# Optimization experiments

Hardware: AMD Instinct MI355X
Metric: run time of the kernel (lower is better)

The kernel has to match this reference:

```python
import jax, jax.numpy as jnp
import numpy as np

H, D, L, G = 4, 32, 2, 512   # heads, head_dim, conv layers, num graphs
HC = H * D                    # hidden_channels = 128


def _mlp3(x, ws, bs):
    # PyG-style MLP, 3 layers, relu between (no act after last), dropout=0
    for i in range(3):
        x = x @ ws[i] + bs[i]
        if i < 2:
            x = jax.nn.relu(x)
    return x


def _attend(q_dst, k_src, v_src, edge, a_rel_et, m_rel_et, p_rel_et, n_dst):
    """One HGTConv edge-type: relation transform, per-dst segment softmax, scatter.
    q_dst: [Nd,H,D], k_src/v_src: [Ns,H,D], edge: [2,E] (src,dst)."""
    src, dst = edge[0], edge[1]
    k_t = jnp.einsum('nhd,hde->nhe', k_src, a_rel_et)   # relation-specific key
    v_t = jnp.einsum('nhd,hde->nhe', v_src, m_rel_et)   # relation-specific value
    alpha = (q_dst[dst] * k_t[src]).sum(-1) * p_rel_et / jnp.sqrt(jnp.float32(D))  # [E,H]
    amax = jax.ops.segment_max(alpha, dst, num_segments=n_dst)
    amax = jnp.where(jnp.isfinite(amax), amax, 0.0)      # nodes with no in-edges
    ex = jnp.exp(alpha - amax[dst])
    den = jax.ops.segment_sum(ex, dst, num_segments=n_dst)
    w = ex / den[dst]                                    # segment softmax weights
    out = jax.ops.segment_sum(v_t[src] * w[..., None], dst, num_segments=n_dst)
    return out.reshape(n_dst, HC)


def _forward(x_var, x_con, mlp_in_w, mlp_in_b,
             mlp_out_w0, mlp_out_b0, mlp_out_w1, mlp_out_b1, mlp_out_w2, mlp_out_b2,
             k_w, k_b, q_w, q_b, v_w, v_b, a_w, a_b, skip,
             a_rel, m_rel, p_rel, edge_vc, edge_cv, batch_var):
    Nv, Nc = x_var.shape[0], x_con.shape[0]
    # per-node-type input MLPs (nt 0 = variable, nt 1 = constraint)
    xs = [_mlp3(x_var, mlp_in_w[0], mlp_in_b[0]),
          _mlp3(x_con, mlp_in_w[1], mlp_in_b[1])]
    ns = [Nv, Nc]
    for l in range(L):  # HGTConv layers
        k = [(xs[t] @ k_w[l, t] + k_b[l, t]).reshape(ns[t], H, D) for t in (0, 1)]
        q = [(xs[t] @ q_w[l, t] + q_b[l, t]).reshape(ns[t], H, D) for t in (0, 1)]
        v = [(xs[t] @ v_w[l, t] + v_b[l, t]).reshape(ns[t], H, D) for t in (0, 1)]
        # edge type 0: variable -> constraint ; edge type 1: constraint -> variable
        agg_con = _attend(q[1], k[0], v[0], edge_vc, a_rel[l, 0], m_rel[l, 0], p_rel[l, 0], Nc)
        agg_var = _attend(q[0], k[1], v[1], edge_cv, a_rel[l, 1], m_rel[l, 1], p_rel[l, 1], Nv)
        # group='mean' over incoming edge types (one per dst type here), then a_lin + gated skip
        new_xs = []
        for t, agg in ((0, agg_var), (1, agg_con)):
            out = jax.nn.gelu(agg, approximate=False) @ a_w[l, t] + a_b[l, t]
            g = jax.nn.sigmoid(skip[l, t])
            new_xs.append(g * out + (1.0 - g) * xs[t])
        xs = new_xs
    # output head on 'variable' nodes: MLP -> softmax(dim=1) -> global mean pool
    logits = _mlp3(xs[0], [mlp_out_w0, mlp_out_w1, mlp_out_w2], [mlp_out_b0, mlp_out_b1, mlp_out_b2])
    probs = jax.nn.softmax(logits, axis=1)
    summ = jax.ops.segment_sum(probs, batch_var, num_segments=G)
    cnt = jax.ops.segment_sum(jnp.ones((xs[0].shape[0],), probs.dtype), batch_var, num_segments=G)
    return summ / jnp.maximum(cnt, 1.0)[:, None]


def setup_inputs() -> dict:
    key = jax.random.key(0)
    ks = jax.random.split(key, 24)
    Nv = Nc = 50000
    E = 400000
    s = 1.0 / np.sqrt(HC)  # fan-in scale for hidden-width linears
    sd = 1.0 / np.sqrt(D)
    inp = {
        'x_var': jax.random.normal(ks[0], (Nv, HC), jnp.float32),
        'x_con': jax.random.normal(ks[1], (Nc, HC), jnp.float32),
        'mlp_in_w': jax.random.normal(ks[2], (2, 3, HC, HC), jnp.float32) * s,
        'mlp_in_b': jnp.zeros((2, 3, HC), jnp.float32),
        'mlp_out_w0': jax.random.normal(ks[3], (HC, HC), jnp.float32) * s,
        'mlp_out_b0': jnp.zeros((HC,), jnp.float32),
        'mlp_out_w1': jax.random.normal(ks[4], (HC, HC), jnp.float32) * s,
        'mlp_out_b1': jnp.zeros((HC,), jnp.float32),
        'mlp_out_w2': jax.random.normal(ks[5], (HC, 2), jnp.float32) * s,
        'mlp_out_b2': jnp.zeros((2,), jnp.float32),
        'k_w': jax.random.normal(ks[6], (L, 2, HC, HC), jnp.float32) * s,
        'k_b': jnp.zeros((L, 2, HC), jnp.float32),
        'q_w': jax.random.normal(ks[7], (L, 2, HC, HC), jnp.float32) * s,
        'q_b': jnp.zeros((L, 2, HC), jnp.float32),
        'v_w': jax.random.normal(ks[8], (L, 2, HC, HC), jnp.float32) * s,
        'v_b': jnp.zeros((L, 2, HC), jnp.float32),
        'a_w': jax.random.normal(ks[9], (L, 2, HC, HC), jnp.float32) * s,
        'a_b': jnp.zeros((L, 2, HC), jnp.float32),
        'skip': jnp.ones((L, 2), jnp.float32),
        'a_rel': jax.random.normal(ks[10], (L, 2, H, D, D), jnp.float32) * sd,
        'm_rel': jax.random.normal(ks[11], (L, 2, H, D, D), jnp.float32) * sd,
        'p_rel': jnp.ones((L, 2, H), jnp.float32),
        'edge_vc': jnp.stack([jax.random.randint(ks[12], (E,), 0, Nv, jnp.int32),
                              jax.random.randint(ks[13], (E,), 0, Nc, jnp.int32)]),
        'edge_cv': jnp.stack([jax.random.randint(ks[14], (E,), 0, Nc, jnp.int32),
                              jax.random.randint(ks[15], (E,), 0, Nv, jnp.int32)]),
        'batch_var': jnp.sort(jax.random.randint(ks[16], (Nv,), 0, G, jnp.int32)),
    }
    return inp


def reference(x_var, x_con, mlp_in_w, mlp_in_b,
              mlp_out_w0, mlp_out_b0, mlp_out_w1, mlp_out_b1, mlp_out_w2, mlp_out_b2,
              k_w, k_b, q_w, q_b, v_w, v_b, a_w, a_b, skip,
              a_rel, m_rel, p_rel, edge_vc, edge_cv, batch_var):
    return _forward(x_var, x_con, mlp_in_w, mlp_in_b,
                    mlp_out_w0, mlp_out_b0, mlp_out_w1, mlp_out_b1, mlp_out_w2, mlp_out_b2,
                    k_w, k_b, q_w, q_b, v_w, v_b, a_w, a_b, skip,
                    a_rel, m_rel, p_rel, edge_vc, edge_cv, batch_var)
```

## Files before the change

kernel.cpp:

```cpp
#include <hip/hip_runtime.h>
#include <cstddef>
#include <cstdint>

typedef __attribute__((ext_vector_type(8))) short short8;
typedef __attribute__((ext_vector_type(4))) float float4v;
typedef __attribute__((ext_vector_type(2))) float float2v;
typedef __attribute__((ext_vector_type(2))) __bf16 bf162;

__device__ __forceinline__ float bf2f_lo(unsigned int u) {
    union { unsigned int i; float f; } v; v.i = u << 16; return v.f;
}
__device__ __forceinline__ float bf2f_hi(unsigned int u) {
    union { unsigned int i; float f; } v; v.i = u & 0xFFFF0000u; return v.f;
}
__device__ __forceinline__ unsigned short f2bf(float f) {
    union { float f; unsigned int i; } v; v.f = f;
    unsigned int x = v.i;
    unsigned int r = (x + 0x7FFFu + ((x >> 16) & 1u)) >> 16;
    return (unsigned short)r;
}
__device__ __forceinline__ float geluf(float x) {
    return 0.5f * x * (1.0f + erff(x * 0.70710678118654752f));
}
__device__ __forceinline__ float dot2bf(unsigned int a, unsigned int b, float c) {
#if defined(__has_builtin) && __has_builtin(__builtin_amdgcn_fdot2_f32_bf16)
    union U { unsigned int u; bf162 v; };
    U ua, ub; ua.u = a; ub.u = b;
    return __builtin_amdgcn_fdot2_f32_bf16(ua.v, ub.v, c, false);
#else
    return c + bf2f_lo(a) * bf2f_lo(b) + bf2f_hi(a) * bf2f_hi(b);
#endif
}
__device__ __forceinline__ unsigned int gate_pack(unsigned int nu, unsigned int ou,
                                                  float2v g2, float2v og2) {
    float2v n = {bf2f_lo(nu), bf2f_hi(nu)};
    float2v o = {bf2f_lo(ou), bf2f_hi(ou)};
    float2v r = n * g2 + o * og2;
    return (unsigned int)f2bf(r.x) | ((unsigned int)f2bf(r.y) << 16);
}

__global__ void k_zero(int* __restrict__ p, int n) {
    int i = blockIdx.x * 256 + threadIdx.x;
    if (i < n) p[i] = 0;
}

__global__ void k_swz(const float* __restrict__ mlp_in_w, const float* __restrict__ q_w,
                      const float* __restrict__ a_w, const float* __restrict__ mow0,
                      const float* __restrict__ mow1, const float* __restrict__ mow2,
                      const float* __restrict__ kw, const float* __restrict__ kb,
                      const float* __restrict__ vw, const float* __restrict__ vb,
                      const float* __restrict__ arel, const float* __restrict__ mrel,
                      const float* __restrict__ prel,
                      unsigned short* __restrict__ Wswz, float* __restrict__ Bkv) {
    int idx = blockIdx.y;
    int f = blockIdx.x * 256 + threadIdx.x;
    if (idx == 25) {
        if (f >= 1024) return;
        int lt = f >> 8, c = f & 255;
        int sec = c >> 7, cc = c & 127, h = cc >> 5, e = cc & 31;
        const float* B = sec ? vb : kb;
        const float* R = sec ? mrel : arel;
        float scale = sec ? 1.f : prel[lt * 4 + h] * 0.17677669529663687f;
        const float* rp = R + (size_t)(lt * 4 + h) * 1024 + e;
        const float* bp = B + lt * 128 + h * 32;
        float s = 0.f;
        #pragma unroll 8
        for (int d = 0; d < 32; ++d) s += bp[d] * rp[(size_t)d * 32];
        Bkv[lt * 256 + c] = s * scale;
        return;
    }
    if (f >= 16384) return;
    int j = f & 7, l = (f >> 3) & 63, t = (f >> 9) & 7, sb = f >> 12;
    int k = sb * 32 + (l >> 4) * 8 + j;
    int n = t * 16 + (l & 15);
    float val;
    if (idx < 6)        val = mlp_in_w[(size_t)idx * 16384 + (size_t)k * 128 + n];
    else if (idx < 10)  val = q_w[(size_t)(idx - 6) * 16384 + (size_t)k * 128 + n];
    else if (idx < 14)  val = a_w[(size_t)(idx - 10) * 16384 + (size_t)k * 128 + n];
    else if (idx == 14) val = mow0[(size_t)k * 128 + n];
    else if (idx == 15) val = mow1[(size_t)k * 128 + n];
    else if (idx < 24) {
        int u = idx - 16, lt = u >> 1, sec = u & 1;
        int h = n >> 5, e = n & 31;
        const float* W = sec ? vw : kw;
        const float* R = sec ? mrel : arel;
        float scale = sec ? 1.f : prel[lt * 4 + h] * 0.17677669529663687f;
        const float* rp = R + (size_t)(lt * 4 + h) * 1024 + e;
        const float* wp = W + (size_t)lt * 16384 + (size_t)k * 128 + h * 32;
        float s = 0.f;
        #pragma unroll 8
        for (int d = 0; d < 32; ++d) s += wp[d] * rp[(size_t)d * 32];
        val = s * scale;
    } else val = (n < 2) ? mow2[(size_t)k * 2 + n] : 0.f;
    Wswz[(size_t)idx * 16384 + f] = f2bf(val);
}

__device__ __forceinline__ void mfma32(const short8 av[4], const unsigned short* __restrict__ Bu,
                                       float4v acc[8]) {
    #pragma unroll
    for (int s = 0; s < 4; ++s)
        #pragma unroll
        for (int t = 0; t < 8; ++t) {
            short8 bv = *(const short8*)(Bu + (s * 8 + t) * 512);
            acc[t] = __builtin_amdgcn_mfma_f32_16x16x32_bf16(av[s], bv, acc[t], 0, 0, 0);
        }
}

__global__ __launch_bounds__(256) void k_mlp3qkv(
    const float* __restrict__ Xa, const float* __restrict__ Xb,
    const unsigned short* __restrict__ Wswz, const float* __restrict__ mlp_in_b,
    const float* __restrict__ q_b, const float* __restrict__ Bkv,
    unsigned short* __restrict__ curS, unsigned short* __restrict__ Qs,
    unsigned short* __restrict__ KVs, int NT, int Nv) {
    __shared__ unsigned short lds[4][16][136];
    const int lane = threadIdx.x & 63, wave = threadIdx.x >> 6;
    const int quad = lane >> 4, mrow = lane & 15;
    const int mbase = blockIdx.x * 64 + wave * 16;
    if (mbase >= NT) return;
    const bool first = mbase < Nv;
    const float* bs = mlp_in_b + (first ? 0 : 384);
    const int ub = first ? 0 : 3;
    const int lt = first ? 0 : 1;
    int r0 = mbase + mrow; if (r0 >= NT) r0 = NT - 1;
    const float* ap = ((r0 < Nv) ? (Xa + (size_t)r0 * 128)
                                 : (Xb + (size_t)(r0 - Nv) * 128)) + quad * 8;
    short8 av[4];
    #pragma unroll
    for (int s = 0; s < 4; ++s) {
        float4 f0 = *(const float4*)(ap + s * 32);
        float4 f1 = *(const float4*)(ap + s * 32 + 4);
        short8 a;
        a[0] = (short)f2bf(f0.x); a[1] = (short)f2bf(f0.y);
        a[2] = (short)f2bf(f0.z); a[3] = (short)f2bf(f0.w);
        a[4] = (short)f2bf(f1.x); a[5] = (short)f2bf(f1.y);
        a[6] = (short)f2bf(f1.z); a[7] = (short)f2bf(f1.w);
        av[s] = a;
    }
    #pragma unroll
    for (int layer = 0; layer < 3; ++layer) {
        const unsigned short* Bu = Wswz + (size_t)(ub + layer) * 16384 + lane * 8;
        float4v acc[8];
        #pragma unroll
        for (int t = 0; t < 8; ++t) acc[t] = (float4v){0.f, 0.f, 0.f, 0.f};
        mfma32(av, Bu, acc);
        const float* b = bs + layer * 128;
        bool relu = layer < 2;
        #pragma unroll
        for (int t = 0; t < 8; ++t) {
            int col = t * 16 + mrow;
            float bb = b[col];
            #pragma unroll
            for (int r = 0; r < 4; ++r) {
                float v = acc[t][r] + bb;
                if (relu) v = fmaxf(v, 0.f);
                lds[wave][quad * 4 + r][col] = f2bf(v);
            }
        }
        #pragma unroll
        for (int s = 0; s < 4; ++s)
            av[s] = *(const short8*)&lds[wave][mrow][s * 32 + quad * 8];
    }
    {
        int row = mbase + mrow;
        if (row < NT) {
            #pragma unroll
            for (int s = 0; s < 4; ++s)
                *(uint4*)(curS + (size_t)row * 128 + quad * 8 + s * 32) = *(uint4*)&av[s];
        }
    }
    #pragma unroll
    for (int u = 0; u < 3; ++u) {
        int unit = (u == 0) ? (6 + lt) : (16 + lt * 2 + (u - 1));
        const unsigned short* Bu = Wswz + (size_t)unit * 16384 + lane * 8;
        float4v acc[8];
        #pragma unroll
        for (int t = 0; t < 8; ++t) acc[t] = (float4v){0.f, 0.f, 0.f, 0.f};
        mfma32(av, Bu, acc);
        const float* bias = (u == 0) ? (q_b + lt * 128) : (Bkv + lt * 256 + (u - 1) * 128);
        unsigned short* C = (u == 0) ? Qs : KVs;
        const int ldC = (u == 0) ? 128 : 256;
        const int cb = (u == 0) ? 0 : (u - 1) * 128;
        #pragma unroll
        for (int t = 0; t < 8; ++t) {
            int col = t * 16 + mrow;
            float b = bias[col];
            #pragma unroll
            for (int r = 0; r < 4; ++r) {
                int row = mbase + quad * 4 + r;
                if (row < NT) C[(size_t)row * ldC + cb + col] = f2bf(acc[t][r] + b);
            }
        }
    }
}

__global__ __launch_bounds__(256) void k_alinqkv(
    const unsigned short* __restrict__ Aagg, const unsigned short* __restrict__ Wswz,
    const float* __restrict__ a_b, const float* __restrict__ skipP,
    const float* __restrict__ q_b, const float* __restrict__ Bkv,
    unsigned short* __restrict__ curS, unsigned short* __restrict__ Qs,
    unsigned short* __restrict__ KVs, int NT, int Nv, int l) {
    __shared__ unsigned short lds[4][16][136];
    const int lane = threadIdx.x & 63, wave = threadIdx.x >> 6;
    const int quad = lane >> 4, mrow = lane & 15;
    const int mbase = blockIdx.x * 64 + wave * 16;
    if (mbase >= NT) return;
    const int type = (mbase >= Nv) ? 1 : 0;
    const int ltA = l * 2 + type;
    const int ltQ = (l + 1) * 2 + type;
    int r0 = mbase + mrow; if (r0 >= NT) r0 = NT - 1;
    const unsigned short* ap = Aagg + (size_t)r0 * 128 + quad * 8;
    short8 av[4];
    #pragma unroll
    for (int s = 0; s < 4; ++s) av[s] = *(const short8*)(ap + s * 32);
    {
        const unsigned short* Bu = Wswz + (size_t)(10 + ltA) * 16384 + lane * 8;
        float4v acc[8];
        #pragma unroll
        for (int t = 0; t < 8; ++t) acc[t] = (float4v){0.f, 0.f, 0.f, 0.f};
        mfma32(av, Bu, acc);
        const float* b = a_b + ltA * 128;
        #pragma unroll
        for (int t = 0; t < 8; ++t) {
            int col = t * 16 + mrow;
            float bb = b[col];
            #pragma unroll
            for (int r = 0; r < 4; ++r)
                lds[wave][quad * 4 + r][col] = f2bf(acc[t][r] + bb);
        }
    }
    {
        float gg = 1.f / (1.f + __expf(-skipP[ltA]));
        float2v g2 = {gg, gg}, og2 = {1.f - gg, 1.f - gg};
        int row = mbase + mrow;
        bool ok = row < NT;
        size_t rbase = (size_t)(ok ? row : 0) * 128;
        #pragma unroll
        for (int s = 0; s < 4; ++s) {
            short8 nv = *(const short8*)&lds[wave][mrow][s * 32 + quad * 8];
            uint4 nu = *(uint4*)&nv;
            uint4 ou = *(const uint4*)(curS + rbase + quad * 8 + s * 32);
            uint4 res;
            res.x = gate_pack(nu.x, ou.x, g2, og2);
            res.y = gate_pack(nu.y, ou.y, g2, og2);
            res.z = gate_pack(nu.z, ou.z, g2, og2);
            res.w = gate_pack(nu.w, ou.w, g2, og2);
            if (ok) *(uint4*)(curS + (size_t)row * 128 + quad * 8 + s * 32) = res;
            av[s] = *(short8*)&res;
        }
    }
    #pragma unroll
    for (int u = 0; u < 3; ++u) {
        int unit = (u == 0) ? (6 + ltQ) : (16 + ltQ * 2 + (u - 1));
        const unsigned short* Bu = Wswz + (size_t)unit * 16384 + lane * 8;
        float4v acc[8];
        #pragma unroll
        for (int t = 0; t < 8; ++t) acc[t] = (float4v){0.f, 0.f, 0.f, 0.f};
        mfma32(av, Bu, acc);
        const float* bias = (u == 0) ? (q_b + ltQ * 128) : (Bkv + ltQ * 256 + (u - 1) * 128);
        unsigned short* C = (u == 0) ? Qs : KVs;
        const int ldC = (u == 0) ? 128 : 256;
        const int cb = (u == 0) ? 0 : (u - 1) * 128;
        #pragma unroll
        for (int t = 0; t < 8; ++t) {
            int col = t * 16 + mrow;
            float b = bias[col];
            #pragma unroll
            for (int r = 0; r < 4; ++r) {
                int row = mbase + quad * 4 + r;
                if (row < NT) C[(size_t)row * ldC + cb + col] = f2bf(acc[t][r] + b);
            }
        }
    }
}

__global__ __launch_bounds__(256) void k_alinhead(
    const unsigned short* __restrict__ Aagg, const unsigned short* __restrict__ Wswz,
    const float* __restrict__ a_b, const float* __restrict__ skipP,
    const unsigned short* __restrict__ curS,
    const float* __restrict__ mob0, const float* __restrict__ mob1,
    const float* __restrict__ mob2, const int* __restrict__ batch,
    int N, int G, float* __restrict__ gsum, float* __restrict__ gcnt) {
    __shared__ unsigned short lds[4][16][136];
    __shared__ float sb[64][3];
    const int lane = threadIdx.x & 63, wave = threadIdx.x >> 6;
    const int quad = lane >> 4, mrow = lane & 15;
    const int tix = threadIdx.x;
    for (int i = tix; i < 192; i += 256) ((float*)sb)[i] = 0.f;
    __syncthreads();
    const int mbase = blockIdx.x * 64 + wave * 16;
    int bbase = blockIdx.x * 64; if (bbase >= N) bbase = N - 1;
    const int bmin = batch[bbase];
    if (mbase < N) {
        int r0 = mbase + mrow; if (r0 >= N) r0 = N - 1;
        const unsigned short* ap = Aagg + (size_t)r0 * 128 + quad * 8;
        short8 av[4];
        #pragma unroll
        for (int s = 0; s < 4; ++s) av[s] = *(const short8*)(ap + s * 32);
        {
            const unsigned short* Bu = Wswz + (size_t)12 * 16384 + lane * 8;
            float4v acc[8];
            #pragma unroll
            for (int t = 0; t < 8; ++t) acc[t] = (float4v){0.f, 0.f, 0.f, 0.f};
            mfma32(av, Bu, acc);
            const float* b = a_b + 2 * 128;
            #pragma unroll
            for (int t = 0; t < 8; ++t) {
                int col = t * 16 + mrow;
                float bb = b[col];
                #pragma unroll
                for (int r = 0; r < 4; ++r)
                    lds[wave][quad * 4 + r][col] = f2bf(acc[t][r] + bb);
            }
        }
        {
            float gg = 1.f / (1.f + __expf(-skipP[2]));
            float2v g2 = {gg, gg}, og2 = {1.f - gg, 1.f - gg};
            size_t rbase = (size_t)r0 * 128;
            #pragma unroll
            for (int s = 0; s < 4; ++s) {
                short8 nv = *(const short8*)&lds[wave][mrow][s * 32 + quad * 8];
                uint4 nu = *(uint4*)&nv;
                uint4 ou = *(const uint4*)(curS + rbase + quad * 8 + s * 32);
                uint4 res;
                res.x = gate_pack(nu.x, ou.x, g2, og2);
                res.y = gate_pack(nu.y, ou.y, g2, og2);
                res.z = gate_pack(nu.z, ou.z, g2, og2);
                res.w = gate_pack(nu.w, ou.w, g2, og2);
                av[s] = *(short8*)&res;
            }
        }
        #pragma unroll
        for (int layer = 0; layer < 2; ++layer) {
            const unsigned short* Bu = Wswz + (size_t)(14 + layer) * 16384 + lane * 8;
            float4v acc[8];
            #pragma unroll
            for (int t = 0; t < 8; ++t) acc[t] = (float4v){0.f, 0.f, 0.f, 0.f};
            mfma32(av, Bu, acc);
            const float* b = layer ? mob1 : mob0;
            #pragma unroll
            for (int t = 0; t < 8; ++t) {
                int col = t * 16 + mrow;
                float bb = b[col];
                #pragma unroll
                for (int r = 0; r < 4; ++r)
                    lds[wave][quad * 4 + r][col] = f2bf(fmaxf(acc[t][r] + bb, 0.f));
            }
            #pragma unroll
            for (int s = 0; s < 4; ++s)
                av[s] = *(const short8*)&lds[wave][mrow][s * 32 + quad * 8];
        }
        float4v lg = (float4v){0.f, 0.f, 0.f, 0.f};
        #pragma unroll
        for (int s = 0; s < 4; ++s) {
            short8 bv = *(const short8*)(Wswz + (size_t)24 * 16384 + (size_t)(s * 8) * 512 + lane * 8);
            lg = __builtin_amdgcn_mfma_f32_16x16x32_bf16(av[s], bv, lg, 0, 0, 0);
        }
        float4v lgo;
        #pragma unroll
        for (int r = 0; r < 4; ++r) lgo[r] = __shfl_xor(lg[r], 1);
        if (mrow == 0) {
            #pragma unroll
            for (int r = 0; r < 4; ++r) {
                int row = mbase + quad * 4 + r;
                if (row < N) {
                    float l0 = lg[r] + mob2[0];
                    float l1 = lgo[r] + mob2[1];
                    float mm = fmaxf(l0, l1);
                    float e0 = __expf(l0 - mm), e1 = __expf(l1 - mm);
                    float inv = 1.f / (e0 + e1);
                    int b = batch[row];
                    int rel = b - bmin;
                    if (rel >= 0 && rel < 64) {
                        atomicAdd(&sb[rel][0], e0 * inv);
                        atomicAdd(&sb[rel][1], e1 * inv);
                        atomicAdd(&sb[rel][2], 1.f);
                    } else {
                        atomicAdd(&gsum[b * 2 + 0], e0 * inv);
                        atomicAdd(&gsum[b * 2 + 1], e1 * inv);
                        atomicAdd(&gcnt[b], 1.f);
                    }
                }
            }
        }
    }
    __syncthreads();
    for (int i = tix; i < 64; i += 256) {
        float c = sb[i][2];
        if (c != 0.f && bmin + i < G) {
            atomicAdd(&gsum[(bmin + i) * 2 + 0], sb[i][0]);
            atomicAdd(&gsum[(bmin + i) * 2 + 1], sb[i][1]);
            atomicAdd(&gcnt[bmin + i], c);
        }
    }
}

__global__ void k_hist2(const int* __restrict__ evc, const int* __restrict__ ecv, int E,
                        int* __restrict__ deg, int Nv) {
    int e = blockIdx.x * 256 + threadIdx.x;
    if (e >= E) return;
    if (blockIdx.y == 0) atomicAdd(&deg[Nv + evc[E + e]], 1);
    else                 atomicAdd(&deg[ecv[E + e]], 1);
}
__global__ void k_scan_block(const int* __restrict__ deg, int n, int* __restrict__ off,
                             int* __restrict__ partials) {
    __shared__ int s[256];
    int i = blockIdx.x * 256 + threadIdx.x;
    s[threadIdx.x] = (i < n) ? deg[i] : 0;
    __syncthreads();
    for (int d = 1; d < 256; d <<= 1) {
        int t = (threadIdx.x >= d) ? s[threadIdx.x - d] : 0;
        __syncthreads();
        s[threadIdx.x] += t;
        __syncthreads();
    }
    if (i < n) off[i + 1] = s[threadIdx.x];
    if (threadIdx.x == 255) partials[blockIdx.x] = s[255];
}
__global__ void k_scan_partials(int* __restrict__ partials, int nb) {
    __shared__ int s[512];
    s[threadIdx.x] = (threadIdx.x < nb) ? partials[threadIdx.x] : 0;
    __syncthreads();
    for (int d = 1; d < 512; d <<= 1) {
        int t = (threadIdx.x >= d) ? s[threadIdx.x - d] : 0;
        __syncthreads();
        s[threadIdx.x] += t;
        __syncthreads();
    }
    if (threadIdx.x < nb) partials[threadIdx.x] = s[threadIdx.x];
}
__global__ void k_scan_add(int* __restrict__ off, int* __restrict__ cur,
                           const int* __restrict__ partials, int n) {
    int i = blockIdx.x * 256 + threadIdx.x;
    if (i == 0) { off[0] = 0; cur[0] = 0; }
    if (i < n) {
        int b = i >> 8;
        int v = off[i + 1] + ((b > 0) ? partials[b - 1] : 0);
        off[i + 1] = v;
        cur[i + 1] = v;
    }
}
__global__ void k_scatter2(const int* __restrict__ evc, const int* __restrict__ ecv, int E,
                           int* __restrict__ cur, int Nv, int* __restrict__ srcAll) {
    int e = blockIdx.x * 256 + threadIdx.x;
    if (e >= E) return;
    if (blockIdx.y == 0) {
        int d = Nv + evc[E + e];
        int pos = atomicAdd(&cur[d], 1);
        srcAll[pos] = evc[e];
    } else {
        int d = ecv[E + e];
        int pos = atomicAdd(&cur[d], 1);
        srcAll[pos] = Nv + ecv[e];
    }
}

__global__ __launch_bounds__(256) void k_agg(
    const unsigned short* __restrict__ Q, const unsigned short* __restrict__ KV,
    const int* __restrict__ off, const int* __restrict__ csrc,
    unsigned short* __restrict__ out, int NT) {
    int dst = blockIdx.x * 4 + (threadIdx.x >> 6);
    int lane = threadIdx.x & 63;
    if (dst >= NT) return;
    const int g = lane >> 4, w = lane & 15;
    int2 se = *(const int2*)(off + dst);
    int s0 = se.x, s1 = se.y;
    uint4 qr = *(const uint4*)(Q + (size_t)dst * 128 + w * 8);
    float2v a0 = {0.f, 0.f}, a1 = {0.f, 0.f}, a2 = {0.f, 0.f}, a3 = {0.f, 0.f};
    float den = 0.f;
    int j = s0 + g;
    uint4 kr = {0, 0, 0, 0}, vr = {0, 0, 0, 0};
    bool have = j < s1;
    if (have) {
        const unsigned short* kv = KV + (size_t)csrc[j] * 256 + w * 8;
        kr = *(const uint4*)kv;
        vr = *(const uint4*)(kv + 128);
    }
    while (have) {
        int jn = j + 4;
        bool haveN = jn < s1;
        uint4 krn = kr, vrn = vr;
        if (haveN) {
            const unsigned short* kv = KV + (size_t)csrc[jn] * 256 + w * 8;
            krn = *(const uint4*)kv;
            vrn = *(const uint4*)(kv + 128);
        }
        float t = dot2bf(kr.x, qr.x, 0.f);
        t = dot2bf(kr.y, qr.y, t);
        t = dot2bf(kr.z, qr.z, t);
        t = dot2bf(kr.w, qr.w, t);
        t += __shfl_xor(t, 1);
        t += __shfl_xor(t, 2);
        t = fminf(fmaxf(t, -30.f), 30.f);
        float p = __expf(t);
        den += p;
        float2v pv = {p, p};
        a0 += pv * (float2v){bf2f_lo(vr.x), bf2f_hi(vr.x)};
        a1 += pv * (float2v){bf2f_lo(vr.y), bf2f_hi(vr.y)};
        a2 += pv * (float2v){bf2f_lo(vr.z), bf2f_hi(vr.z)};
        a3 += pv * (float2v){bf2f_lo(vr.w), bf2f_hi(vr.w)};
        kr = krn; vr = vrn; j = jn; have = haveN;
    }
    den += __shfl_xor(den, 16); den += __shfl_xor(den, 32);
    a0.x += __shfl_xor(a0.x, 16); a0.x += __shfl_xor(a0.x, 32);
    a0.y += __shfl_xor(a0.y, 16); a0.y += __shfl_xor(a0.y, 32);
    a1.x += __shfl_xor(a1.x, 16); a1.x += __shfl_xor(a1.x, 32);
    a1.y += __shfl_xor(a1.y, 16); a1.y += __shfl_xor(a1.y, 32);
    a2.x += __shfl_xor(a2.x, 16); a2.x += __shfl_xor(a2.x, 32);
    a2.y += __shfl_xor(a2.y, 16); a2.y += __shfl_xor(a2.y, 32);
    a3.x += __shfl_xor(a3.x, 16); a3.x += __shfl_xor(a3.x, 32);
    a3.y += __shfl_xor(a3.y, 16); a3.y += __shfl_xor(a3.y, 32);
    float inv = (s1 > s0) ? 1.f / den : 0.f;
    float2v r = a0;
    if (g == 1) r = a1;
    if (g == 2) r = a2;
    if (g == 3) r = a3;
    float r0 = geluf(r.x * inv), r1 = geluf(r.y * inv);
    unsigned int o = (unsigned int)f2bf(r0) | ((unsigned int)f2bf(r1) << 16);
    *(unsigned int*)(out + (size_t)dst * 128 + w * 8 + g * 2) = o;
}

__global__ void k_finalize(const float* __restrict__ gsum, const float* __restrict__ gcnt,
                           float* __restrict__ out, int n) {
    int i = blockIdx.x * 256 + threadIdx.x;
    if (i < n) out[i] = gsum[i] / fmaxf(gcnt[i >> 1], 1.f);
}

extern "C" void kernel_launch(void* const* d_in, const int* in_sizes, int n_in,
                              void* d_out, int out_size, void* d_ws, size_t ws_size,
                              hipStream_t stream) {
    const float* x_var    = (const float*)d_in[0];
    const float* x_con    = (const float*)d_in[1];
    const float* mlp_in_w = (const float*)d_in[2];
    const float* mlp_in_b = (const float*)d_in[3];
    const float* mow0 = (const float*)d_in[4];
    const float* mob0 = (const float*)d_in[5];
    const float* mow1 = (const float*)d_in[6];
    const float* mob1 = (const float*)d_in[7];
    const float* mow2 = (const float*)d_in[8];
    const float* mob2 = (const float*)d_in[9];
    const float* k_w  = (const float*)d_in[10];
    const float* k_b  = (const float*)d_in[11];
    const float* q_w  = (const float*)d_in[12];
    const float* q_b  = (const float*)d_in[13];
    const float* v_w  = (const float*)d_in[14];
    const float* v_b  = (const float*)d_in[15];
    const float* a_w  = (const float*)d_in[16];
    const float* a_b  = (const float*)d_in[17];
    const float* skipP = (const float*)d_in[18];
    const float* a_rel = (const float*)d_in[19];
    const float* m_rel = (const float*)d_in[20];
    const float* p_rel = (const float*)d_in[21];
    const int* edge_vc = (const int*)d_in[22];
    const int* edge_cv = (const int*)d_in[23];
    const int* batch   = (const int*)d_in[24];

    const int Nv = in_sizes[0] / 128;
    const int Nc = in_sizes[1] / 128;
    const int E  = in_sizes[22] / 2;
    const int G  = out_size / 2;
    const int NT = Nv + Nc;

    float* fbase = (float*)d_ws;
    size_t fo = 0;
    auto falloc = [&](size_t n) { float* p = fbase + fo; fo += n; return p; };
    float* Bkv  = falloc(4 * 256);
    float* gsum = falloc((size_t)G * 2);
    float* gcnt = falloc((size_t)G);

    unsigned short* bbase = (unsigned short*)(fbase + fo);
    size_t bo = 0;
    auto balloc = [&](size_t n) { unsigned short* p = bbase + bo; bo += n; return p; };
    unsigned short* Wswz = balloc((size_t)25 * 16384);
    unsigned short* curS = balloc((size_t)NT * 128);
    unsigned short* Qs   = balloc((size_t)NT * 128);
    unsigned short* KVs  = balloc((size_t)NT * 256);

    int* ibase = (int*)(bbase + bo);
    size_t io = 0;
    auto ialloc = [&](size_t n) { int* p = ibase + io; io += n; return p; };
    int* offAll = ialloc((size_t)NT + 1);
    int* curAll = ialloc((size_t)NT + 1);
    int* srcAll = ialloc((size_t)E * 2);
    int* deg    = ialloc((size_t)NT);
    int* partials = ialloc(512);

    size_t need = (char*)(ibase + io) - (char*)d_ws;
    if (need > ws_size) return;

    const int eb  = (E + 255) / 256;
    const int nzb = (NT + 255) / 256;
    const int gNT = (NT + 63) / 64;
    const int gNv = (Nv + 63) / 64;

    k_zero<<<nzb, 256, 0, stream>>>(deg, NT);
    k_hist2<<<dim3(eb, 2), 256, 0, stream>>>(edge_vc, edge_cv, E, deg, Nv);
    k_scan_block<<<nzb, 256, 0, stream>>>(deg, NT, offAll, partials);
    k_scan_partials<<<1, 512, 0, stream>>>(partials, nzb);
    k_scan_add<<<nzb, 256, 0, stream>>>(offAll, curAll, partials, NT);
    k_scatter2<<<dim3(eb, 2), 256, 0, stream>>>(edge_vc, edge_cv, E, curAll, Nv, srcAll);

    k_swz<<<dim3(64, 26), 256, 0, stream>>>(mlp_in_w, q_w, a_w, mow0, mow1, mow2,
                                            k_w, k_b, v_w, v_b, a_rel, m_rel, p_rel,
                                            Wswz, Bkv);
    k_zero<<<(G * 3 + 255) / 256, 256, 0, stream>>>((int*)gsum, G * 3);

    k_mlp3qkv<<<gNT, 256, 0, stream>>>(x_var, x_con, Wswz, mlp_in_b, q_b, Bkv,
                                       curS, Qs, KVs, NT, Nv);
    k_agg<<<(NT + 3) / 4, 256, 0, stream>>>(Qs, KVs, offAll, srcAll, Qs, NT);
    k_alinqkv<<<gNT, 256, 0, stream>>>(Qs, Wswz, a_b, skipP, q_b, Bkv,
                                       curS, Qs, KVs, NT, Nv, 0);
    k_agg<<<(NT + 3) / 4, 256, 0, stream>>>(Qs, KVs, offAll, srcAll, Qs, NT);
    k_alinhead<<<gNv, 256, 0, stream>>>(Qs, Wswz, a_b, skipP, curS,
                                        mob0, mob1, mob2, batch, Nv, G, gsum, gcnt);
    k_finalize<<<(G * 2 + 255) / 256, 256, 0, stream>>>(gsum, gcnt, (float*)d_out, G * 2);
}
```

Before: 525.4 us.

## Process 64 rows per wave in dense MFMA kernels to reuse weight fragments

Each wave in the three dense GEMM-chain kernels now handles four 16-row groups (64 rows) rather than one. Every B-fragment load is reused across four MFMAs, cutting global/L2 weight traffic per row. Blocks shrink to 128 threads, and the grid is split per node type so a tile never mixes variable and constraint rows. The cost is higher register pressure (16 A fragments plus 4 accumulators) and fewer waves overall, which may reduce occupancy and latency hiding.

```diff
diff --git a/kernel.cpp b/kernel.cpp
--- a/kernel.cpp
+++ b/kernel.cpp
@@ -95,230 +95,177 @@
     Wswz[(size_t)idx * 16384 + f] = f2bf(val);
 }
 
-__device__ __forceinline__ void mfma32(const short8 av[4], const unsigned short* __restrict__ Bu,
-                                       float4v acc[8]) {
-    #pragma unroll
-    for (int s = 0; s < 4; ++s)
-        #pragma unroll
-        for (int t = 0; t < 8; ++t) {
-            short8 bv = *(const short8*)(Bu + (s * 8 + t) * 512);
-            acc[t] = __builtin_amdgcn_mfma_f32_16x16x32_bf16(av[s], bv, acc[t], 0, 0, 0);
-        }
-}
-
-__global__ __launch_bounds__(256) void k_mlp3qkv(
+__device__ __forceinline__ void unit_t(const short8 av[4][4], const unsigned short* __restrict__ Bu,
+                                       int t, float4v acc[4]) {
+    #pragma unroll
+    for (int rg = 0; rg < 4; ++rg) acc[rg] = (float4v){0.f, 0.f, 0.f, 0.f};
+    #pragma unroll
+    for (int s = 0; s < 4; ++s) {
+        short8 bv = *(const short8*)(Bu + (s * 8 + t) * 512);
+        #pragma unroll
+        for (int rg = 0; rg < 4; ++rg)
+            acc[rg] = __builtin_amdgcn_mfma_f32_16x16x32_bf16(av[rg][s], bv, acc[rg], 0, 0, 0);
+    }
+}
+
+__global__ __launch_bounds__(128) void k_mlp3qkv(
     const float* __restrict__ Xa, const float* __restrict__ Xb,
     const unsigned short* __restrict__ Wswz, const float* __restrict__ mlp_in_b,
     const float* __restrict__ q_b, const float* __restrict__ Bkv,
     unsigned short* __restrict__ curS, unsigned short* __restrict__ Qs,
-    unsigned short* __restrict__ KVs, int NT, int Nv) {
-    __shared__ unsigned short lds[4][16][136];
+    unsigned short* __restrict__ KVs, int NT, int Nv, int Bv) {
+    __shared__ unsigned short lds[2][64][136];
     const int lane = threadIdx.x & 63, wave = threadIdx.x >> 6;
     const int quad = lane >> 4, mrow = lane & 15;
-    const int mbase = blockIdx.x * 64 + wave * 16;
-    if (mbase >= NT) return;
-    const bool first = mbase < Nv;
-    const float* bs = mlp_in_b + (first ? 0 : 384);
-    const int ub = first ? 0 : 3;
-    const int lt = first ? 0 : 1;
-    int r0 = mbase + mrow; if (r0 >= NT) r0 = NT - 1;
-    const float* ap = ((r0 < Nv) ? (Xa + (size_t)r0 * 128)
-                                 : (Xb + (size_t)(r0 - Nv) * 128)) + quad * 8;
-    short8 av[4];
-    #pragma unroll
-    for (int s = 0; s < 4; ++s) {
-        float4 f0 = *(const float4*)(ap + s * 32);
-        float4 f1 = *(const float4*)(ap + s * 32 + 4);
-        short8 a;
-        a[0] = (short)f2bf(f0.x); a[1] = (short)f2bf(f0.y);
-        a[2] = (short)f2bf(f0.z); a[3] = (short)f2bf(f0.w);
-        a[4] = (short)f2bf(f1.x); a[5] = (short)f2bf(f1.y);
-        a[6] = (short)f2bf(f1.z); a[7] = (short)f2bf(f1.w);
-        av[s] = a;
+    int bx = blockIdx.x;
+    int base, end, type;
+    if (bx < Bv) { base = bx * 128; end = Nv; type = 0; }
+    else         { base = Nv + (bx - Bv) * 128; end = NT; type = 1; }
+    const int mbase = base + wave * 64;
+    if (mbase >= end) return;
+    const float* bs = mlp_in_b + type * 384;
+    const int ub = type * 3;
+    const int lt = type;
+    int rows[4];
+    #pragma unroll
+    for (int rg = 0; rg < 4; ++rg) {
+        int r = mbase + rg * 16 + mrow;
+        rows[rg] = (r < end) ? r : end - 1;
+    }
+    short8 av[4][4];
+    #pragma unroll
+    for (int rg = 0; rg < 4; ++rg) {
+        const float* ap = (type == 0 ? Xa + (size_t)rows[rg] * 128
+                                     : Xb + (size_t)(rows[rg] - Nv) * 128) + quad * 8;
+        #pragma unroll
+        for (int s = 0; s < 4; ++s) {
+            float4 f0 = *(const float4*)(ap + s * 32);
+            float4 f1 = *(const float4*)(ap + s * 32 + 4);
+            short8 a;
+            a[0] = (short)f2bf(f0.x); a[1] = (short)f2bf(f0.y);
+            a[2] = (short)f2bf(f0.z); a[3] = (short)f2bf(f0.w);
+            a[4] = (short)f2bf(f1.x); a[5] = (short)f2bf(f1.y);
+            a[6] = (short)f2bf(f1.z); a[7] = (short)f2bf(f1.w);
+            av[rg][s] = a;
+        }
     }
     #pragma unroll
     for (int layer = 0; layer < 3; ++layer) {
         const unsigned short* Bu = Wswz + (size_t)(ub + layer) * 16384 + lane * 8;
-        float4v acc[8];
-        #pragma unroll
-        for (int t = 0; t < 8; ++t) acc[t] = (float4v){0.f, 0.f, 0.f, 0.f};
-        mfma32(av, Bu, acc);
         const float* b = bs + layer * 128;
         bool relu = layer < 2;
         #pragma unroll
         for (int t = 0; t < 8; ++t) {
+            float4v acc[4];
+            unit_t(av, Bu, t, acc);
             int col = t * 16 + mrow;
             float bb = b[col];
             #pragma unroll
-            for (int r = 0; r < 4; ++r) {
-                float v = acc[t][r] + bb;
-                if (relu) v = fmaxf(v, 0.f);
-                lds[wave][quad * 4 + r][col] = f2bf(v);
-            }
-        }
-        #pragma unroll
-        for (int s = 0; s < 4; ++s)
-            av[s] = *(const short8*)&lds[wave][mrow][s * 32 + quad * 8];
-    }
-    {
-        int row = mbase + mrow;
-        if (row < NT) {
+            for (int rg = 0; rg < 4; ++rg)
+                #pragma unroll
+                for (int r = 0; r < 4; ++r) {
+                    float v = acc[rg][r] + bb;
+                    if (relu) v = fmaxf(v, 0.f);
+                    lds[wave][rg * 16 + quad * 4 + r][col] = f2bf(v);
+                }
+        }
+        #pragma unroll
+        for (int rg = 0; rg < 4; ++rg)
             #pragma unroll
             for (int s = 0; s < 4; ++s)
-                *(uint4*)(curS + (size_t)row * 128 + quad * 8 + s * 32) = *(uint4*)&av[s];
+                av[rg][s] = *(const short8*)&lds[wave][rg * 16 + mrow][s * 32 + quad * 8];
+    }
+    #pragma unroll
+    for (int rg = 0; rg < 4; ++rg) {
+        int row = mbase + rg * 16 + mrow;
+        if (row < end) {
+            #pragma unroll
+            for (int s = 0; s < 4; ++s)
+                *(uint4*)(curS + (size_t)row * 128 + quad * 8 + s * 32) = *(uint4*)&av[rg][s];
         }
     }
     #pragma unroll
     for (int u = 0; u < 3; ++u) {
         int unit = (u == 0) ? (6 + lt) : (16 + lt * 2 + (u - 1));
         const unsigned short* Bu = Wswz + (size_t)unit * 16384 + lane * 8;
-        float4v acc[8];
-        #pragma unroll
-        for (int t = 0; t < 8; ++t) acc[t] = (float4v){0.f, 0.f, 0.f, 0.f};
-        mfma32(av, Bu, acc);
         const float* bias = (u == 0) ? (q_b + lt * 128) : (Bkv + lt * 256 + (u - 1) * 128);
         unsigned short* C = (u == 0) ? Qs : KVs;
         const int ldC = (u == 0) ? 128 : 256;
         const int cb = (u == 0) ? 0 : (u - 1) * 128;
         #pragma unroll
         for (int t = 0; t < 8; ++t) {
+            float4v acc[4];
+            unit_t(av, Bu, t, acc);
             int col = t * 16 + mrow;
             float b = bias[col];
             #pragma unroll
-            for (int r = 0; r < 4; ++r) {
-                int row = mbase + quad * 4 + r;
-                if (row < NT) C[(size_t)row * ldC + cb + col] = f2bf(acc[t][r] + b);
-            }
-        }
-    }
-}
-
-__global__ __launch_bounds__(256) void k_alinqkv(
+            for (int rg = 0; rg < 4; ++rg)
+                #pragma unroll
+                for (int r = 0; r < 4; ++r) {
+                    int row = mbase + rg * 16 + quad * 4 + r;
+                    if (row < end) C[(size_t)row * ldC + cb + col] = f2bf(acc[rg][r] + b);
+                }
+        }
+    }
+}
+
+__global__ __launch_bounds__(128) void k_alinqkv(
     const unsigned short* __restrict__ Aagg, const unsigned short* __restrict__ Wswz,
     const float* __restrict__ a_b, const float* __restrict__ skipP,
     const float* __restrict__ q_b, const float* __restrict__ Bkv,
     unsigned short* __restrict__ curS, unsigned short* __restrict__ Qs,
-    unsigned short* __restrict__ KVs, int NT, int Nv, int l) {
-    __shared__ unsigned short lds[4][16][136];
+    unsigned short* __restrict__ KVs, int NT, int Nv, int Bv, int l) {
+    __shared__ unsigned short lds[2][64][136];
     const int lane = threadIdx.x & 63, wave = threadIdx.x >> 6;
     const int quad = lane >> 4, mrow = lane & 15;
-    const int mbase = blockIdx.x * 64 + wave * 16;
-    if (mbase >= NT) return;
-    const int type = (mbase >= Nv) ? 1 : 0;
+    int bx = blockIdx.x;
+    int base, end, type;
+    if (bx < Bv) { base = bx * 128; end = Nv; type = 0; }
+    else         { base = Nv + (bx - Bv) * 128; end = NT; type = 1; }
+    const int mbase = base + wave * 64;
+    if (mbase >= end) return;
     const int ltA = l * 2 + type;
     const int ltQ = (l + 1) * 2 + type;
-    int r0 = mbase + mrow; if (r0 >= NT) r0 = NT - 1;
-    const unsigned short* ap = Aagg + (size_t)r0 * 128 + quad * 8;
-    short8 av[4];
-    #pragma unroll
-    for (int s = 0; s < 4; ++s) av[s] = *(const short8*)(ap + s * 32);
+    int rows[4];
+    #pragma unroll
+    for (int rg = 0; rg < 4; ++rg) {
+        int r = mbase + rg * 16 + mrow;
+        rows[rg] = (r < end) ? r : end - 1;
+    }
+    short8 av[4][4];
+    #pragma unroll
+    for (int rg = 0; rg < 4; ++rg) {
+        const unsigned short* ap = Aagg + (size_t)rows[rg] * 128 + quad * 8;
+        #pragma unroll
+        for (int s = 0; s < 4; ++s) av[rg][s] = *(const short8*)(ap + s * 32);
+    }
     {
         const unsigned short* Bu = Wswz + (size_t)(10 + ltA) * 16384 + lane * 8;
-        float4v acc[8];
-        #pragma unroll
-        for (int t = 0; t < 8; ++t) acc[t] = (float4v){0.f, 0.f, 0.f, 0.f};
-        mfma32(av, Bu, acc);
         const float* b = a_b + ltA * 128;
         #pragma unroll
         for (int t = 0; t < 8; ++t) {
+            float4v acc[4];
+            unit_t(av, Bu, t, acc);
             int col = t * 16 + mrow;
             float bb = b[col];
             #pragma unroll
-            for (int r = 0; r < 4; ++r)
-                lds[wave][quad * 4 + r][col] = f2bf(acc[t][r] + bb);
+            for (int rg = 0; rg < 4; ++rg)
+                #pragma unroll
+                for (int r = 0; r < 4; ++r)
+                    lds[wave][rg * 16 + quad * 4 + r][col] = f2bf(acc[rg][r] + bb);
         }
     }
     {
         float gg = 1.f / (1.f + __expf(-skipP[ltA]));
         float2v g2 = {gg, gg}, og2 = {1.f - gg, 1.f - gg};
-        int row = mbase + mrow;
-        bool ok = row < NT;
-        size_t rbase = (size_t)(ok ? row : 0) * 128;
-        #pragma unroll
-        for (int s = 0; s < 4; ++s) {
-            short8 nv = *(const short8*)&lds[wave][mrow][s * 32 + quad * 8];
-            uint4 nu = *(uint4*)&nv;
-            uint4 ou = *(const uint4*)(curS + rbase + quad * 8 + s * 32);
-            uint4 res;
-            res.x = gate_pack(nu.x, ou.x, g2, og2);
-            res.y = gate_pack(nu.y, ou.y, g2, og2);
-            res.z = gate_pack(nu.z, ou.z, g2, og2);
-            res.w = gate_pack(nu.w, ou.w, g2, og2);
-            if (ok) *(uint4*)(curS + (size_t)row * 128 + quad * 8 + s * 32) = res;
-            av[s] = *(short8*)&res;
-        }
-    }
-    #pragma unroll
-    for (int u = 0; u < 3; ++u) {
-        int unit = (u == 0) ? (6 + ltQ) : (16 + ltQ * 2 + (u - 1));
-        const unsigned short* Bu = Wswz + (size_t)unit * 16384 + lane * 8;
-        float4v acc[8];
-        #pragma unroll
-        for (int t = 0; t < 8; ++t) acc[t] = (float4v){0.f, 0.f, 0.f, 0.f};
-        mfma32(av, Bu, acc);
-        const float* bias = (u == 0) ? (q_b + ltQ * 128) : (Bkv + ltQ * 256 + (u - 1) * 128);
-        unsigned short* C = (u == 0) ? Qs : KVs;
-        const int ldC = (u == 0) ? 128 : 256;
-        const int cb = (u == 0) ? 0 : (u - 1) * 128;
-        #pragma unroll
-        for (int t = 0; t < 8; ++t) {
-            int col = t * 16 + mrow;
-            float b = bias[col];
-            #pragma unroll
-            for (int r = 0; r < 4; ++r) {
-                int row = mbase + quad * 4 + r;
-                if (row < NT) C[(size_t)row * ldC + cb + col] = f2bf(acc[t][r] + b);
-            }
-        }
-    }
-}
-
-__global__ __launch_bounds__(256) void k_alinhead(
-    const unsigned short* __restrict__ Aagg, const unsigned short* __restrict__ Wswz,
-    const float* __restrict__ a_b, const float* __restrict__ skipP,
-    const unsigned short* __restrict__ curS,
-    const float* __restrict__ mob0, const float* __restrict__ mob1,
-    const float* __restrict__ mob2, const int* __restrict__ batch,
-    int N, int G, float* __restrict__ gsum, float* __restrict__ gcnt) {
-    __shared__ unsigned short lds[4][16][136];
-    __shared__ float sb[64][3];
-    const int lane = threadIdx.x & 63, wave = threadIdx.x >> 6;
-    const int quad = lane >> 4, mrow = lane & 15;
-    const int tix = threadIdx.x;
-    for (int i = tix; i < 192; i += 256) ((float*)sb)[i] = 0.f;
-    __syncthreads();
-    const int mbase = blockIdx.x * 64 + wave * 16;
-    int bbase = blockIdx.x * 64; if (bbase >= N) bbase = N - 1;
-    const int bmin = batch[bbase];
-    if (mbase < N) {
-        int r0 = mbase + mrow; if (r0 >= N) r0 = N - 1;
-        const unsigned short* ap = Aagg + (size_t)r0 * 128 + quad * 8;
-        short8 av[4];
-        #pragma unroll
-        for (int s = 0; s < 4; ++s) av[s] = *(const short8*)(ap + s * 32);
-        {
-            const unsigned short* Bu = Wswz + (size_t)12 * 16384 + lane * 8;
-            float4v acc[8];
-            #pragma unroll
-            for (int t = 0; t < 8; ++t) acc[t] = (float4v){0.f, 0.f, 0.f, 0.f};
-            mfma32(av, Bu, acc);
-            const float* b = a_b + 2 * 128;
-            #pragma unroll
-            for (int t = 0; t < 8; ++t) {
-                int col = t * 16 + mrow;
-                float bb = b[col];
-                #pragma unroll
-                for (int r = 0; r < 4; ++r)
-                    lds[wave][quad * 4 + r][col] = f2bf(acc[t][r] + bb);
-            }
-        }
-        {
-            float gg = 1.f / (1.f + __expf(-skipP[2]));
-            float2v g2 = {gg, gg}, og2 = {1.f - gg, 1.f - gg};
-            size_t rbase = (size_t)r0 * 128;
+        #pragma unroll
+        for (int rg = 0; rg < 4; ++rg) {
+            int row = mbase + rg * 16 + mrow;
+            bool ok = row < end;
+            size_t rbase = (size_t)rows[rg] * 128;
             #pragma unroll
             for (int s = 0; s < 4; ++s) {
-                short8 nv = *(const short8*)&lds[wave][mrow][s * 32 + quad * 8];
+                short8 nv = *(const short8*)&lds[wave][rg * 16 + mrow][s * 32 + quad * 8];
                 uint4 nu = *(uint4*)&nv;
                 uint4 ou = *(const uint4*)(curS + rbase + quad * 8 + s * 32);
                 uint4 res;
@@ -326,65 +273,168 @@
                 res.y = gate_pack(nu.y, ou.y, g2, og2);
                 res.z = gate_pack(nu.z, ou.z, g2, og2);
                 res.w = gate_pack(nu.w, ou.w, g2, og2);
-                av[s] = *(short8*)&res;
+                if (ok) *(uint4*)(curS + (size_t)row * 128 + quad * 8 + s * 32) = res;
+                av[rg][s] = *(short8*)&res;
+            }
+        }
+    }
+    #pragma unroll
+    for (int u = 0; u < 3; ++u) {
+        int unit = (u == 0) ? (6 + ltQ) : (16 + ltQ * 2 + (u - 1));
+        const unsigned short* Bu = Wswz + (size_t)unit * 16384 + lane * 8;
+        const float* bias = (u == 0) ? (q_b + ltQ * 128) : (Bkv + ltQ * 256 + (u - 1) * 128);
+        unsigned short* C = (u == 0) ? Qs : KVs;
+        const int ldC = (u == 0) ? 128 : 256;
+        const int cb = (u == 0) ? 0 : (u - 1) * 128;
+        #pragma unroll
+        for (int t = 0; t < 8; ++t) {
+            float4v acc[4];
+            unit_t(av, Bu, t, acc);
+            int col = t * 16 + mrow;
+            float b = bias[col];
+            #pragma unroll
+            for (int rg = 0; rg < 4; ++rg)
+                #pragma unroll
+                for (int r = 0; r < 4; ++r) {
+                    int row = mbase + rg * 16 + quad * 4 + r;
+                    if (row < end) C[(size_t)row * ldC + cb + col] = f2bf(acc[rg][r] + b);
+                }
+        }
+    }
+}
+
+__global__ __launch_bounds__(128) void k_alinhead(
+    const unsigned short* __restrict__ Aagg, const unsigned short* __restrict__ Wswz,
+    const float* __restrict__ a_b, const float* __restrict__ skipP,
+    const unsigned short* __restrict__ curS,
+    const float* __restrict__ mob0, const float* __restrict__ mob1,
+    const float* __restrict__ mob2, const int* __restrict__ batch,
+    int N, int G, float* __restrict__ gsum, float* __restrict__ gcnt) {
+    __shared__ unsigned short lds[2][64][136];
+    __shared__ float sb[64][3];
+    const int lane = threadIdx.x & 63, wave = threadIdx.x >> 6;
+    const int quad = lane >> 4, mrow = lane & 15;
+    const int tix = threadIdx.x;
+    for (int i = tix; i < 192; i += 128) ((float*)sb)[i] = 0.f;
+    __syncthreads();
+    const int mbase = blockIdx.x * 128 + wave * 64;
+    int bb0 = blockIdx.x * 128; if (bb0 >= N) bb0 = N - 1;
+    const int bmin = batch[bb0];
+    if (mbase < N) {
+        int rows[4];
+        #pragma unroll
+        for (int rg = 0; rg < 4; ++rg) {
+            int r = mbase + rg * 16 + mrow;
+            rows[rg] = (r < N) ? r : N - 1;
+        }
+        short8 av[4][4];
+        #pragma unroll
+        for (int rg = 0; rg < 4; ++rg) {
+            const unsigned short* ap = Aagg + (size_t)rows[rg] * 128 + quad * 8;
+            #pragma unroll
+            for (int s = 0; s < 4; ++s) av[rg][s] = *(const short8*)(ap + s * 32);
+        }
+        {
+            const unsigned short* Bu = Wswz + (size_t)12 * 16384 + lane * 8;
+            const float* b = a_b + 2 * 128;
+            #pragma unroll
+            for (int t = 0; t < 8; ++t) {
+                float4v acc[4];
+                unit_t(av, Bu, t, acc);
+                int col = t * 16 + mrow;
+                float bbv = b[col];
+                #pragma unroll
+                for (int rg = 0; rg < 4; ++rg)
+                    #pragma unroll
+                    for (int r = 0; r < 4; ++r)
+                        lds[wave][rg * 16 + quad * 4 + r][col] = f2bf(acc[rg][r] + bbv);
+            }
+        }
+        {
+            float gg = 1.f / (1.f + __expf(-skipP[2]));
+            float2v g2 = {gg, gg}, og2 = {1.f - gg, 1.f - gg};
+            #pragma unroll
+            for (int rg = 0; rg < 4; ++rg) {
+                size_t rbase = (size_t)rows[rg] * 128;
+                #pragma unroll
+                for (int s = 0; s < 4; ++s) {
+                    short8 nv = *(const short8*)&lds[wave][rg * 16 + mrow][s * 32 + quad * 8];
+                    uint4 nu = *(uint4*)&nv;
+                    uint4 ou = *(const uint4*)(curS + rbase + quad * 8 + s * 32);
+                    uint4 res;
+                    res.x = gate_pack(nu.x, ou.x, g2, og2);
+                    res.y = gate_pack(nu.y, ou.y, g2, og2);
+                    res.z = gate_pack(nu.z, ou.z, g2, og2);
+                    res.w = gate_pack(nu.w, ou.w, g2, og2);
+                    av[rg][s] = *(short8*)&res;
+                }
             }
         }
         #pragma unroll
         for (int layer = 0; layer < 2; ++layer) {
             const unsigned short* Bu = Wswz + (size_t)(14 + layer) * 16384 + lane * 8;
-            float4v acc[8];
-            #pragma unroll
-            for (int t = 0; t < 8; ++t) acc[t] = (float4v){0.f, 0.f, 0.f, 0.f};
-            mfma32(av, Bu, acc);
             const float* b = layer ? mob1 : mob0;
             #pragma unroll
             for (int t = 0; t < 8; ++t) {
+                float4v acc[4];
+                unit_t(av, Bu, t, acc);
                 int col = t * 16 + mrow;
-                float bb = b[col];
-                #pragma unroll
-                for (int r = 0; r < 4; ++r)
-                    lds[wave][quad * 4 + r][col] = f2bf(fmaxf(acc[t][r] + bb, 0.f));
+                float bbv = b[col];
+                #pragma unroll
+                for (int rg = 0; rg < 4; ++rg)
+                    #pragma unroll
+                    for (int r = 0; r < 4; ++r)
+                        lds[wave][rg * 16 + quad * 4 + r][col] = f2bf(fmaxf(acc[rg][r] + bbv, 0.f));
             }
             #pragma unroll
-            for (int s = 0; s < 4; ++s)
-                av[s] = *(const short8*)&lds[wave][mrow][s * 32 + quad * 8];
-        }
-        float4v lg = (float4v){0.f, 0.f, 0.f, 0.f};
+            for (int rg = 0; rg < 4; ++rg)
+                #pragma unroll
+                for (int s = 0; s < 4; ++s)
+                    av[rg][s] = *(const short8*)&lds[wave][rg * 16 + mrow][s * 32 + quad * 8];
+        }
+        float4v lg[4];
+        #pragma unroll
+        for (int rg = 0; rg < 4; ++rg) lg[rg] = (float4v){0.f, 0.f, 0.f, 0.f};
         #pragma unroll
         for (int s = 0; s < 4; ++s) {
             short8 bv = *(const short8*)(Wswz + (size_t)24 * 16384 + (size_t)(s * 8) * 512 + lane * 8);
-            lg = __builtin_amdgcn_mfma_f32_16x16x32_bf16(av[s], bv, lg, 0, 0, 0);
-        }
-        float4v lgo;
-        #pragma unroll
-        for (int r = 0; r < 4; ++r) lgo[r] = __shfl_xor(lg[r], 1);
-        if (mrow == 0) {
-            #pragma unroll
-            for (int r = 0; r < 4; ++r) {
-                int row = mbase + quad * 4 + r;
-                if (row < N) {
-                    float l0 = lg[r] + mob2[0];
-                    float l1 = lgo[r] + mob2[1];
-                    float mm = fmaxf(l0, l1);
-                    float e0 = __expf(l0 - mm), e1 = __expf(l1 - mm);
-                    float inv = 1.f / (e0 + e1);
-                    int b = batch[row];
-                    int rel = b - bmin;
-                    if (rel >= 0 && rel < 64) {
-                        atomicAdd(&sb[rel][0], e0 * inv);
-                        atomicAdd(&sb[rel][1], e1 * inv);
-                        atomicAdd(&sb[rel][2], 1.f);
-                    } else {
-                        atomicAdd(&gsum[b * 2 + 0], e0 * inv);
-                        atomicAdd(&gsum[b * 2 + 1], e1 * inv);
-                        atomicAdd(&gcnt[b], 1.f);
+            #pragma unroll
+            for (int rg = 0; rg < 4; ++rg)
+                lg[rg] = __builtin_amdgcn_mfma_f32_16x16x32_bf16(av[rg][s], bv, lg[rg], 0, 0, 0);
+        }
+        #pragma unroll
+        for (int rg = 0; rg < 4; ++rg) {
+            float4v lgo;
+            #pragma unroll
+            for (int r = 0; r < 4; ++r) lgo[r] = __shfl_xor(lg[rg][r], 1);
+            if (mrow == 0) {
+                #pragma unroll
+                for (int r = 0; r < 4; ++r) {
+                    int row = mbase + rg * 16 + quad * 4 + r;
+                    if (row < N) {
+                        float l0 = lg[rg][r] + mob2[0];
+                        float l1 = lgo[r] + mob2[1];
+                        float mm = fmaxf(l0, l1);
+                        float e0 = __expf(l0 - mm), e1 = __expf(l1 - mm);
+                        float inv = 1.f / (e0 + e1);
+                        int b = batch[row];
+                        int rel = b - bmin;
+                        if (rel >= 0 && rel < 64) {
+                            atomicAdd(&sb[rel][0], e0 * inv);
+                            atomicAdd(&sb[rel][1], e1 * inv);
+                            atomicAdd(&sb[rel][2], 1.f);
+                        } else {
+                            atomicAdd(&gsum[b * 2 + 0], e0 * inv);
+                            atomicAdd(&gsum[b * 2 + 1], e1 * inv);
+                            atomicAdd(&gcnt[b], 1.f);
+                        }
                     }
                 }
             }
         }
     }
     __syncthreads();
-    for (int i = tix; i < 64; i += 256) {
+    for (int i = tix; i < 64; i += 128) {
         float c = sb[i][2];
         if (c != 0.f && bmin + i < G) {
             atomicAdd(&gsum[(bmin + i) * 2 + 0], sb[i][0]);
@@ -589,8 +639,8 @@
 
     const int eb  = (E + 255) / 256;
     const int nzb = (NT + 255) / 256;
-    const int gNT = (NT + 63) / 64;
-    const int gNv = (Nv + 63) / 64;
+    const int Bv  = (Nv + 127) / 128;
+    const int Bc  = (Nc + 127) / 128;
 
     k_zero<<<nzb, 256, 0, stream>>>(deg, NT);
     k_hist2<<<dim3(eb, 2), 256, 0, stream>>>(edge_vc, edge_cv, E, deg, Nv);
@@ -604,13 +654,13 @@
                                             Wswz, Bkv);
     k_zero<<<(G * 3 + 255) / 256, 256, 0, stream>>>((int*)gsum, G * 3);
 
-    k_mlp3qkv<<<gNT, 256, 0, stream>>>(x_var, x_con, Wswz, mlp_in_b, q_b, Bkv,
-                                       curS, Qs, KVs, NT, Nv);
+    k_mlp3qkv<<<Bv + Bc, 128, 0, stream>>>(x_var, x_con, Wswz, mlp_in_b, q_b, Bkv,
+                                           curS, Qs, KVs, NT, Nv, Bv);
     k_agg<<<(NT + 3) / 4, 256, 0, stream>>>(Qs, KVs, offAll, srcAll, Qs, NT);
-    k_alinqkv<<<gNT, 256, 0, stream>>>(Qs, Wswz, a_b, skipP, q_b, Bkv,
-                                       curS, Qs, KVs, NT, Nv, 0);
+    k_alinqkv<<<Bv + Bc, 128, 0, stream>>>(Qs, Wswz, a_b, skipP, q_b, Bkv,
+                                           curS, Qs, KVs, NT, Nv, Bv, 0);
     k_agg<<<(NT + 3) / 4, 256, 0, stream>>>(Qs, KVs, offAll, srcAll, Qs, NT);
-    k_alinhead<<<gNv, 256, 0, stream>>>(Qs, Wswz, a_b, skipP, curS,
-                                        mob0, mob1, mob2, batch, Nv, G, gsum, gcnt);
+    k_alinhead<<<Bv, 128, 0, stream>>>(Qs, Wswz, a_b, skipP, curS,
+                                       mob0, mob1, mob2, batch, Nv, G, gsum, gcnt);
     k_finalize<<<(G * 2 + 255) / 256, 256, 0, stream>>>(gsum, gcnt, (float*)d_out, G * 2);
 }
```

New measurement: 691.5 us. 1.32x slower.
